# Kernel tuning notes

Hardware: AMD Instinct MI355X
Metric: run time of the kernel (lower is better)

The kernel has to match this reference:

```python
import jax, jax.numpy as jnp
import numpy as np

N = 20000      # total residues (nodes)
E = 320000     # contact edges
G = 16         # graphs in batch
D_IN = 1280    # ESM embedding dim
H = 256        # hidden channels (1=2=3)
C = 500        # GO classes
EPS = 1e-5


def setup_inputs() -> dict:
    key = jax.random.key(0)
    ks = jax.random.split(key, 16)
    s = 0.02
    return {
        "x": jax.random.normal(ks[0], (N, D_IN), jnp.float32),
        "edge_index": jax.random.randint(ks[1], (2, E), 0, N, jnp.int32),
        "edge_attr": jax.random.uniform(ks[2], (E, 1), jnp.float32),
        "batch": jnp.sort(jax.random.randint(ks[3], (N,), 0, G, jnp.int32)),
        "seq_emb": jax.random.normal(ks[4], (G, D_IN), jnp.float32),
        "W1": jax.random.normal(ks[5], (D_IN, H), jnp.float32) * s,
        "b1": jnp.zeros((H,), jnp.float32),
        "g1": jnp.ones((H,), jnp.float32),
        "be1": jnp.zeros((H,), jnp.float32),
        "W2": jax.random.normal(ks[6], (H, H), jnp.float32) * s,
        "b2": jnp.zeros((H,), jnp.float32),
        "g2": jnp.ones((H,), jnp.float32),
        "be2": jnp.zeros((H,), jnp.float32),
        "W3": jax.random.normal(ks[7], (H, H), jnp.float32) * s,
        "b3": jnp.zeros((H,), jnp.float32),
        "g3": jnp.ones((H,), jnp.float32),
        "be3": jnp.zeros((H,), jnp.float32),
        "fc1_w": jax.random.normal(ks[8], (D_IN, H), jnp.float32) * s,
        "fc1_b": jnp.zeros((H,), jnp.float32),
        "lin_w": jax.random.normal(ks[9], (H, C), jnp.float32) * s,
        "lin_b": jnp.zeros((C,), jnp.float32),
    }


def gcn_conv(x, row, col, ew, W, b):
    # PyG GCNConv: x' = D^{-1/2} (A + I) D^{-1/2} X W + b, with edge weights,
    # self-loops of weight 1, aggregation at target (col).
    xw = x @ W                                             # [N, H]
    deg = jax.ops.segment_sum(ew, col, num_segments=N) + 1.0
    dinv = jax.lax.rsqrt(deg)                              # [N]
    norm = dinv[row] * ew * dinv[col]                      # [E]
    agg = jax.ops.segment_sum(norm[:, None] * xw[row], col, num_segments=N)
    agg = agg + (dinv * dinv)[:, None] * xw                # self-loop term
    return agg + b


def batch_norm(x, g, b):
    # training-mode BN over the node dimension (biased variance, as torch)
    m = jnp.mean(x, axis=0)
    v = jnp.var(x, axis=0)
    return (x - m) * jax.lax.rsqrt(v + EPS) * g + b


def reference(x, edge_index, edge_attr, batch, seq_emb,
              W1, b1, g1, be1, W2, b2, g2, be2, W3, b3, g3, be3,
              fc1_w, fc1_b, lin_w, lin_b):
    row, col = edge_index[0], edge_index[1]
    ew = edge_attr[:, 0]

    h = batch_norm(jax.nn.relu(gcn_conv(x, row, col, ew, W1, b1)), g1, be1)
    h = batch_norm(jax.nn.relu(gcn_conv(h, row, col, ew, W2, b2)), g2, be2)
    h = batch_norm(gcn_conv(h, row, col, ew, W3, b3), g3, be3)

    # global_mean_pool over graphs
    sums = jax.ops.segment_sum(h, batch, num_segments=G)        # [G, H]
    cnt = jax.ops.segment_sum(jnp.ones((h.shape[0],), h.dtype), batch, num_segments=G)
    pooled = sums / jnp.maximum(cnt, 1.0)[:, None]

    y = seq_emb @ fc1_w + fc1_b                                 # [G, H]
    out = pooled + y
    # dropout skipped (eval mode)
    out = out @ lin_w + lin_b                                   # [G, C]
    return jax.nn.sigmoid(out)
```

## Files before the change

### kernel.cpp

```cpp
#include <hip/hip_runtime.h>
#include <hip/hip_bf16.h>
#include <math.h>

#define Nn 20000
#define En 320000
#define Gn 16
#define DINn 1280
#define Hn 256
#define Cn 500
#define EPSn 1e-5f
#define BNB 1024
#define SCB 256
#define SNB ((Nn + SCB - 1) / SCB)

typedef __attribute__((ext_vector_type(8))) short bf16x8;
typedef __attribute__((ext_vector_type(4))) float f32x4;

__device__ __forceinline__ float b2f(ushort u) {
    return __uint_as_float(((unsigned int)u) << 16);
}
__device__ __forceinline__ ushort f2b(float f) {
    __hip_bfloat16 h = __float2bfloat16(f);
    return *reinterpret_cast<ushort*>(&h);
}

#define GLOAD16(g, l) __builtin_amdgcn_global_load_lds( \
    (const __attribute__((address_space(1))) unsigned int*)(g), \
    (__attribute__((address_space(3))) unsigned int*)(l), 16, 0, 0)


__global__ void k_deg(const int* col, const float* ew, float* deg) {
    int e = blockIdx.x * blockDim.x + threadIdx.x;
    if (e < En) atomicAdd(&deg[col[e]], ew[e]);
}

__global__ void k_dinv(const float* deg, float* dinv, float* dinv2) {
    int i = blockIdx.x * blockDim.x + threadIdx.x;
    if (i < Nn) {
        float d = deg[i] + 1.0f;
        float r = rsqrtf(d);
        dinv[i] = r;
        dinv2[i] = 1.0f / d;
    }
}

__global__ void k_norm_count(const int* row, const int* col, const float* ew,
                             const float* dinv, float* normE, int* counts) {
    int e = blockIdx.x * blockDim.x + threadIdx.x;
    if (e < En) {
        int r = row[e], c = col[e];
        normE[e] = dinv[r] * ew[e] * dinv[c];
        atomicAdd(&counts[c], 1);
    }
}


__global__ __launch_bounds__(SCB) void k_scanA(const int* __restrict__ counts,
                                               int* __restrict__ excl,
                                               int* __restrict__ blocksum) {
    __shared__ int sd[SCB];
    int t = threadIdx.x, b = blockIdx.x;
    int i = b * SCB + t;
    int v = (i < Nn) ? counts[i] : 0;
    sd[t] = v;
    __syncthreads();
    #pragma unroll
    for (int o = 1; o < SCB; o <<= 1) {
        int tv = (t >= o) ? sd[t - o] : 0;
        __syncthreads();
        sd[t] += tv;
        __syncthreads();
    }
    if (i < Nn) excl[i] = sd[t] - v;
    if (t == SCB - 1) blocksum[b] = sd[t];
}

__global__ __launch_bounds__(128) void k_scanB(const int* __restrict__ blocksum,
                                               int* __restrict__ blockoff,
                                               int* __restrict__ offsets) {
    __shared__ int sd[128];
    int t = threadIdx.x;
    int v = (t < SNB) ? blocksum[t] : 0;
    sd[t] = v;
    __syncthreads();
    #pragma unroll
    for (int o = 1; o < 128; o <<= 1) {
        int tv = (t >= o) ? sd[t - o] : 0;
        __syncthreads();
        sd[t] += tv;
        __syncthreads();
    }
    if (t < SNB) blockoff[t] = sd[t] - v;
    if (t == SNB - 1) offsets[Nn] = sd[t];
}

__global__ __launch_bounds__(SCB) void k_scanC(const int* __restrict__ excl,
                                               const int* __restrict__ blockoff,
                                               int* __restrict__ offsets,
                                               int* __restrict__ cursor) {
    int b = blockIdx.x;
    int i = b * SCB + threadIdx.x;
    if (i < Nn) {
        int o = excl[i] + blockoff[b];
        offsets[i] = o;
        cursor[i] = o;
    }
}

__global__ void k_fill(const int* row, const int* col, const float* normE,
                       int* cursor, int* csr_row, float* csr_w) {
    int e = blockIdx.x * blockDim.x + threadIdx.x;
    if (e < En) {
        int c = col[e];
        int p = atomicAdd(&cursor[c], 1);
        csr_row[p] = row[e];
        csr_w[p] = normE[e];
    }
}


__global__ void k_gbounds(const int* __restrict__ batch, int* __restrict__ gstart) {
    int i = blockIdx.x * blockDim.x + threadIdx.x;
    if (i >= Nn) return;
    int b = batch[i];
    if (i == 0) {
        for (int g = 0; g <= b; g++) gstart[g] = 0;
    } else {
        int pb = batch[i - 1];
        for (int g = pb + 1; g <= b; g++) gstart[g] = i;
    }
    if (i == Nn - 1) {
        for (int g = b + 1; g <= Gn; g++) gstart[g] = Nn;
    }
}


__global__ __launch_bounds__(256) void k_x2bf(const float* __restrict__ x,
                                              ushort* __restrict__ xb) {
    size_t i = ((size_t)blockIdx.x * blockDim.x + threadIdx.x) * 8;
    const float4* xp = reinterpret_cast<const float4*>(&x[i]);
    float4 a = xp[0], b = xp[1];
    ushort t[8];
    t[0] = f2b(a.x); t[1] = f2b(a.y); t[2] = f2b(a.z); t[3] = f2b(a.w);
    t[4] = f2b(b.x); t[5] = f2b(b.y); t[6] = f2b(b.z); t[7] = f2b(b.w);
    *reinterpret_cast<uint4*>(&xb[i]) = *reinterpret_cast<uint4*>(&t[0]);
}


__global__ __launch_bounds__(256) void k_wt(const float* __restrict__ W,
                                            ushort* __restrict__ WT, int K) {
    __shared__ float tile[32][33];
    int k0 = blockIdx.x * 32, n0 = blockIdx.y * 32;
    int tx = threadIdx.x, ty = threadIdx.y;
    #pragma unroll
    for (int i = 0; i < 32; i += 8)
        tile[ty + i][tx] = W[(size_t)(k0 + ty + i) * Hn + n0 + tx];
    __syncthreads();
    #pragma unroll
    for (int i = 0; i < 32; i += 8)
        WT[(size_t)(n0 + ty + i) * K + k0 + tx] = f2b(tile[tx][ty + i]);
}


__global__ __launch_bounds__(256) void k_wtb(const float* __restrict__ W,
                                             const float* __restrict__ scaleA,
                                             const float* __restrict__ shiftA,
                                             ushort* __restrict__ WT,
                                             float* __restrict__ bv) {
    __shared__ float tile[32][33];
    int k0 = blockIdx.x * 32, n0 = blockIdx.y * 32;
    int tx = threadIdx.x, ty = threadIdx.y;
    #pragma unroll
    for (int i = 0; i < 32; i += 8)
        tile[ty + i][tx] = W[(size_t)(k0 + ty + i) * Hn + n0 + tx];
    __syncthreads();
    float sc = scaleA[k0 + tx], sh = shiftA[k0 + tx];
    #pragma unroll
    for (int i = 0; i < 32; i += 8) {
        float w = tile[tx][ty + i];
        WT[(size_t)(n0 + ty + i) * Hn + k0 + tx] = f2b(w * sc);
        float pb = w * sh;
        #pragma unroll
        for (int o = 16; o > 0; o >>= 1) pb += __shfl_down(pb, o, 32);
        if (tx == 0) atomicAdd(&bv[n0 + ty + i], pb);
    }
}


#define GBM 64
#define GBN 128
#define GBK 64

__global__ __launch_bounds__(256) void k_gemm_bf(
    const ushort* __restrict__ A, const ushort* __restrict__ BT,
    ushort* __restrict__ C, int M, int K, int NBL)
{
    __shared__ ushort Asl[GBM][GBK];
    __shared__ ushort Bsl[GBN][GBK];
    const int id = blockIdx.x;
    const int k8 = id >> 3;
    const int r8 = id & 7;
    const int p = (k8 >> 1) * 8 + r8;
    const int bnk = k8 & 1;
    if (p >= NBL) return;
    const int bm = p * GBM;
    const int bn = bnk * GBN;
    const int tid = threadIdx.x;
    const int lane = tid & 63;
    const int wid = tid >> 6;
    const int wm = wid >> 1, wn = wid & 1;
    const int l15 = lane & 15, l16 = lane >> 4;

    const int lrow = lane >> 3;
    const int lcolb = 16 * ((lane & 7) ^ lrow);

    f32x4 acc[2][4] = {};
    const int nt = K / GBK;

    for (int t = 0; t < nt; t++) {
        const int k0 = t * GBK;
        #pragma unroll
        for (int c = 0; c < 2; c++) {
            int chunk = wid * 2 + c;
            int grow = bm + chunk * 8 + lrow;
            if (grow >= M) grow = M - 1;
            const char* src = (const char*)&A[(size_t)grow * K + k0] + lcolb;
            GLOAD16(src, &Asl[chunk * 8][0]);
        }
        #pragma unroll
        for (int c = 0; c < 4; c++) {
            int chunk = wid * 4 + c;
            int grow = bn + chunk * 8 + lrow;
            const char* src = (const char*)&BT[(size_t)grow * K + k0] + lcolb;
            GLOAD16(src, &Bsl[chunk * 8][0]);
        }
        __syncthreads();

        #pragma unroll
        for (int ks = 0; ks < 2; ks++) {
            bf16x8 afr[2], bfr[4];
            #pragma unroll
            for (int i = 0; i < 2; i++) {
                int r = wm * 32 + i * 16 + l15;
                int cb = (ks * 64 + l16 * 16) ^ ((r & 7) << 4);
                afr[i] = *reinterpret_cast<const bf16x8*>((const char*)&Asl[r][0] + cb);
            }
            #pragma unroll
            for (int j = 0; j < 4; j++) {
                int r = wn * 64 + j * 16 + l15;
                int cb = (ks * 64 + l16 * 16) ^ ((r & 7) << 4);
                bfr[j] = *reinterpret_cast<const bf16x8*>((const char*)&Bsl[r][0] + cb);
            }
            #pragma unroll
            for (int i = 0; i < 2; i++)
                #pragma unroll
                for (int j = 0; j < 4; j++)
                    acc[i][j] = __builtin_amdgcn_mfma_f32_16x16x32_bf16(afr[i], bfr[j], acc[i][j], 0, 0, 0);
        }
        __syncthreads();
    }

    #pragma unroll
    for (int i = 0; i < 2; i++) {
        #pragma unroll
        for (int r = 0; r < 4; r++) {
            int grow = bm + wm * 32 + i * 16 + l16 * 4 + r;
            if (grow < M) {
                #pragma unroll
                for (int j = 0; j < 4; j++)
                    C[(size_t)grow * Hn + bn + wn * 64 + j * 16 + l15] = f2b(acc[i][j][r]);
            }
        }
    }
}


__device__ __forceinline__ void agg_accum(float* acc, float w, const uint4& v) {
    unsigned int u;
    u = v.x; acc[0] += w * b2f((ushort)u); acc[1] += w * b2f((ushort)(u >> 16));
    u = v.y; acc[2] += w * b2f((ushort)u); acc[3] += w * b2f((ushort)(u >> 16));
    u = v.z; acc[4] += w * b2f((ushort)u); acc[5] += w * b2f((ushort)(u >> 16));
    u = v.w; acc[6] += w * b2f((ushort)u); acc[7] += w * b2f((ushort)(u >> 16));
}

__global__ __launch_bounds__(256) void k_agg(const ushort* __restrict__ xw,
                                             const int* __restrict__ offsets,
                                             const int* __restrict__ csr_row,
                                             const float* __restrict__ csr_w,
                                             const float* __restrict__ dinv2,
                                             const float* __restrict__ bias,
                                             const float* __restrict__ bv,
                                             ushort* __restrict__ outp, int do_relu) {
    int node = blockIdx.x * 8 + (threadIdx.x >> 5);
    int l32 = threadIdx.x & 31;
    int s = offsets[node], e = offsets[node + 1];
    const uint4* xw4 = reinterpret_cast<const uint4*>(xw);

    float acc[8] = {};
    float wsum = 0.f;
    int k = s;
    for (; k + 4 <= e; k += 4) {
        int r0 = csr_row[k],     r1 = csr_row[k + 1];
        int r2 = csr_row[k + 2], r3 = csr_row[k + 3];
        float w0 = csr_w[k],     w1 = csr_w[k + 1];
        float w2 = csr_w[k + 2], w3 = csr_w[k + 3];
        uint4 v0 = xw4[(size_t)r0 * 32 + l32];
        uint4 v1 = xw4[(size_t)r1 * 32 + l32];
        uint4 v2 = xw4[(size_t)r2 * 32 + l32];
        uint4 v3 = xw4[(size_t)r3 * 32 + l32];
        wsum += (w0 + w1) + (w2 + w3);
        agg_accum(acc, w0, v0);
        agg_accum(acc, w1, v1);
        agg_accum(acc, w2, v2);
        agg_accum(acc, w3, v3);
    }
    for (; k < e; k++) {
        int r = csr_row[k];
        float w = csr_w[k];
        uint4 v = xw4[(size_t)r * 32 + l32];
        wsum += w;
        agg_accum(acc, w, v);
    }
    float d2 = dinv2[node];
    wsum += d2;
    uint4 vs = xw4[(size_t)node * 32 + l32];
    agg_accum(acc, d2, vs);

    const float4* bp = reinterpret_cast<const float4*>(&bias[l32 * 8]);
    float4 bb0 = bp[0], bb1 = bp[1];
    acc[0] += bb0.x; acc[1] += bb0.y; acc[2] += bb0.z; acc[3] += bb0.w;
    acc[4] += bb1.x; acc[5] += bb1.y; acc[6] += bb1.z; acc[7] += bb1.w;
    if (bv) {
        const float4* vp = reinterpret_cast<const float4*>(&bv[l32 * 8]);
        float4 bv0 = vp[0], bv1 = vp[1];
        acc[0] += wsum * bv0.x; acc[1] += wsum * bv0.y;
        acc[2] += wsum * bv0.z; acc[3] += wsum * bv0.w;
        acc[4] += wsum * bv1.x; acc[5] += wsum * bv1.y;
        acc[6] += wsum * bv1.z; acc[7] += wsum * bv1.w;
    }
    if (do_relu) {
        #pragma unroll
        for (int q = 0; q < 8; q++) acc[q] = fmaxf(acc[q], 0.f);
    }
    uint4 o;
    o.x = (unsigned int)f2b(acc[0]) | ((unsigned int)f2b(acc[1]) << 16);
    o.y = (unsigned int)f2b(acc[2]) | ((unsigned int)f2b(acc[3]) << 16);
    o.z = (unsigned int)f2b(acc[4]) | ((unsigned int)f2b(acc[5]) << 16);
    o.w = (unsigned int)f2b(acc[6]) | ((unsigned int)f2b(acc[7]) << 16);
    reinterpret_cast<uint4*>(outp)[(size_t)node * 32 + l32] = o;
}


__global__ __launch_bounds__(256) void k_bnpart(const ushort* __restrict__ h,
                                                float* __restrict__ partial) {
    int f = threadIdx.x;
    int blk = blockIdx.x;
    float s = 0.0f, ss = 0.0f;
    for (int i = blk; i < Nn; i += BNB) {
        float v = b2f(h[(size_t)i * Hn + f]);
        s += v;
        ss += v * v;
    }
    partial[(size_t)blk * 512 + f] = s;
    partial[(size_t)blk * 512 + 256 + f] = ss;
}

__global__ __launch_bounds__(256) void k_bnred(const float* __restrict__ partial,
                                               float* __restrict__ p2) {
    int f = threadIdx.x;
    int b = blockIdx.x;
    int b0 = b * 64;
    float s = 0.0f, ss = 0.0f;
    for (int j = 0; j < 64; j++) {
        const float* p = &partial[(size_t)(b0 + j) * 512];
        s += p[f];
        ss += p[256 + f];
    }
    p2[b * 512 + f] = s;
    p2[b * 512 + 256 + f] = ss;
}

__global__ void k_bnfinal2(const float* __restrict__ p2, const float* g, const float* be,
                           float* scaleA, float* shiftA) {
    int f = threadIdx.x;
    float s = 0.f, ss = 0.f;
    #pragma unroll
    for (int j = 0; j < 16; j++) {
        s += p2[j * 512 + f];
        ss += p2[j * 512 + 256 + f];
    }
    float mean = s / (float)Nn;
    float var = ss / (float)Nn - mean * mean;
    float a = g[f] * rsqrtf(var + EPSn);
    scaleA[f] = a;
    shiftA[f] = be[f] - mean * a;
}


#define PCH 32

__global__ __launch_bounds__(256) void k_pool2(const ushort* __restrict__ h,
                                               const int* __restrict__ gstart,
                                               const float* __restrict__ scaleA,
                                               const float* __restrict__ shiftA,
                                               float* __restrict__ pooled) {
    int g = blockIdx.x;
    int chunk = blockIdx.y;
    int f = threadIdx.x;
    int s = gstart[g], e = gstart[g + 1];
    int len = e - s;
    if (len <= 0) return;
    int per = (len + PCH - 1) / PCH;
    int cs = s + chunk * per;
    int ce = cs + per; if (ce > e) ce = e;
    if (cs >= ce) return;
    float sc = scaleA[f], sh = shiftA[f];
    float acc = 0.0f;
    for (int i = cs; i < ce; i++)
        acc += b2f(h[(size_t)i * Hn + f]) * sc + sh;
    atomicAdd(&pooled[g * Hn + f], acc);
}


__global__ __launch_bounds__(256) void k_head1part(const float* __restrict__ seq_emb,
                                                   const float* __restrict__ fc1_w,
                                                   float* __restrict__ hpart) {
    int g = blockIdx.x;
    int kc = blockIdx.y;
    int j = threadIdx.x;
    const float* se = &seq_emb[(size_t)g * DINn + kc * 128];
    const float* w = &fc1_w[(size_t)kc * 128 * Hn + j];
    float acc = 0.0f;
    #pragma unroll 8
    for (int k = 0; k < 128; k++)
        acc += se[k] * w[(size_t)k * Hn];
    hpart[((size_t)g * 10 + kc) * Hn + j] = acc;
}

__global__ __launch_bounds__(256) void k_head2f(const float* __restrict__ hpart,
                                                const float* __restrict__ fc1_b,
                                                const float* __restrict__ pooled,
                                                const int* __restrict__ gstart,
                                                const float* __restrict__ lin_w,
                                                const float* __restrict__ lin_b,
                                                float* __restrict__ out) {
    __shared__ float pf[Hn];
    int g = blockIdx.x;
    int half = blockIdx.y;
    int j = threadIdx.x;
    float s = fc1_b[j];
    #pragma unroll
    for (int kc = 0; kc < 10; kc++)
        s += hpart[((size_t)g * 10 + kc) * Hn + j];
    float cntf = fmaxf((float)(gstart[g + 1] - gstart[g]), 1.0f);
    pf[j] = pooled[g * Hn + j] / cntf + s;
    __syncthreads();
    int c = half * 250 + j;
    if (j < 250) {
        float a2 = lin_b[c];
        #pragma unroll 8
        for (int k = 0; k < Hn; k++)
            a2 += pf[k] * lin_w[(size_t)k * Cn + c];
        out[g * Cn + c] = 1.0f / (1.0f + expf(-a2));
    }
}


extern "C" void kernel_launch(void* const* d_in, const int* in_sizes, int n_in,
                              void* d_out, int out_size, void* d_ws, size_t ws_size,
                              hipStream_t stream) {
    const float* x        = (const float*)d_in[0];
    const int*   eidx     = (const int*)d_in[1];
    const float* eattr    = (const float*)d_in[2];
    const int*   batch    = (const int*)d_in[3];
    const float* seq_emb  = (const float*)d_in[4];
    const float* W1 = (const float*)d_in[5];
    const float* b1 = (const float*)d_in[6];
    const float* g1 = (const float*)d_in[7];
    const float* be1 = (const float*)d_in[8];
    const float* W2 = (const float*)d_in[9];
    const float* b2 = (const float*)d_in[10];
    const float* g2 = (const float*)d_in[11];
    const float* be2 = (const float*)d_in[12];
    const float* W3 = (const float*)d_in[13];
    const float* b3 = (const float*)d_in[14];
    const float* g3 = (const float*)d_in[15];
    const float* be3 = (const float*)d_in[16];
    const float* fc1_w = (const float*)d_in[17];
    const float* fc1_b = (const float*)d_in[18];
    const float* lin_w = (const float*)d_in[19];
    const float* lin_b = (const float*)d_in[20];
    float* out = (float*)d_out;

    const int* row = eidx;
    const int* col = eidx + En;

    char* ws = (char*)d_ws;
    size_t off = 0;
    auto alloc = [&](size_t bytes) -> char* {
        char* p = ws + off;
        off += (bytes + 255) & ~(size_t)255;
        return p;
    };
    ushort* xb     = (ushort*)alloc((size_t)Nn * DINn * 2);
    ushort* xwb    = (ushort*)alloc((size_t)Nn * Hn * 2);
    ushort* hb     = (ushort*)alloc((size_t)Nn * Hn * 2);
    char*  zbase   = ws + off;
    float* deg     = (float*)alloc(Nn * 4);
    int*   counts  = (int*)alloc(Nn * 4);
    float* bvA     = (float*)alloc(Hn * 4);
    float* bvB     = (float*)alloc(Hn * 4);
    float* pooled  = (float*)alloc(Gn * Hn * 4);
    size_t zspan   = (size_t)((ws + off) - zbase);
    float* dinv    = (float*)alloc(Nn * 4);
    float* dinv2   = (float*)alloc(Nn * 4);
    float* normE   = (float*)alloc(En * 4);
    int*   offsets = (int*)alloc((Nn + 1) * 4);
    int*   cursor  = (int*)alloc(Nn * 4);
    int*   excl    = (int*)alloc(Nn * 4);
    int*   blocksum= (int*)alloc(SNB * 4);
    int*   blockoff= (int*)alloc(SNB * 4);
    int*   csr_row = (int*)alloc(En * 4);
    float* csr_w   = (float*)alloc(En * 4);
    float* scaleA  = (float*)alloc(Hn * 4);
    float* shiftA  = (float*)alloc(Hn * 4);
    int*   gstart  = (int*)alloc((Gn + 1) * 4);
    float* partial = (float*)alloc((size_t)BNB * 512 * 4);
    float* p2      = (float*)alloc(16 * 512 * 4);
    float* hpart   = (float*)alloc((size_t)Gn * 10 * Hn * 4);
    ushort* W1T    = (ushort*)alloc((size_t)Hn * DINn * 2);
    ushort* W2T    = (ushort*)alloc((size_t)Hn * Hn * 2);
    ushort* W3T    = (ushort*)alloc((size_t)Hn * Hn * 2);

    const int TB = 256;
    const int EB = (En + TB - 1) / TB;
    const int NB = (Nn + TB - 1) / TB;

    hipMemsetAsync(zbase, 0, zspan, stream);
    k_deg<<<EB, TB, 0, stream>>>(col, eattr, deg);
    k_dinv<<<NB, TB, 0, stream>>>(deg, dinv, dinv2);
    k_norm_count<<<EB, TB, 0, stream>>>(row, col, eattr, dinv, normE, counts);
    k_scanA<<<SNB, SCB, 0, stream>>>(counts, excl, blocksum);
    k_scanB<<<1, 128, 0, stream>>>(blocksum, blockoff, offsets);
    k_scanC<<<SNB, SCB, 0, stream>>>(excl, blockoff, offsets, cursor);
    k_fill<<<EB, TB, 0, stream>>>(row, col, normE, cursor, csr_row, csr_w);
    k_gbounds<<<NB, TB, 0, stream>>>(batch, gstart);
    k_x2bf<<<(Nn * DINn / 8) / 256, 256, 0, stream>>>(x, xb);
    k_wt<<<dim3(DINn / 32, Hn / 32), dim3(32, 8), 0, stream>>>(W1, W1T, DINn);

    const int NBL = (Nn + GBM - 1) / GBM;
    const int GGRID = ((NBL * 2 + 15) / 16) * 16;
    const int AGB = Nn / 8;

    k_gemm_bf<<<GGRID, 256, 0, stream>>>(xb, W1T, xwb, Nn, DINn, NBL);
    k_agg<<<AGB, 256, 0, stream>>>(xwb, offsets, csr_row, csr_w, dinv2, b1, nullptr, hb, 1);
    k_bnpart<<<BNB, Hn, 0, stream>>>(hb, partial);
    k_bnred<<<16, Hn, 0, stream>>>(partial, p2);
    k_bnfinal2<<<1, Hn, 0, stream>>>(p2, g1, be1, scaleA, shiftA);

    k_wtb<<<dim3(Hn / 32, Hn / 32), dim3(32, 8), 0, stream>>>(W2, scaleA, shiftA, W2T, bvA);
    k_gemm_bf<<<GGRID, 256, 0, stream>>>(hb, W2T, xwb, Nn, Hn, NBL);
    k_agg<<<AGB, 256, 0, stream>>>(xwb, offsets, csr_row, csr_w, dinv2, b2, bvA, hb, 1);
    k_bnpart<<<BNB, Hn, 0, stream>>>(hb, partial);
    k_bnred<<<16, Hn, 0, stream>>>(partial, p2);
    k_bnfinal2<<<1, Hn, 0, stream>>>(p2, g2, be2, scaleA, shiftA);

    k_wtb<<<dim3(Hn / 32, Hn / 32), dim3(32, 8), 0, stream>>>(W3, scaleA, shiftA, W3T, bvB);
    k_gemm_bf<<<GGRID, 256, 0, stream>>>(hb, W3T, xwb, Nn, Hn, NBL);
    k_agg<<<AGB, 256, 0, stream>>>(xwb, offsets, csr_row, csr_w, dinv2, b3, bvB, hb, 0);
    k_bnpart<<<BNB, Hn, 0, stream>>>(hb, partial);
    k_bnred<<<16, Hn, 0, stream>>>(partial, p2);
    k_bnfinal2<<<1, Hn, 0, stream>>>(p2, g3, be3, scaleA, shiftA);

    k_pool2<<<dim3(Gn, PCH), Hn, 0, stream>>>(hb, gstart, scaleA, shiftA, pooled);
    k_head1part<<<dim3(Gn, 10), Hn, 0, stream>>>(seq_emb, fc1_w, hpart);
    k_head2f<<<dim3(Gn, 2), Hn, 0, stream>>>(hpart, fc1_b, pooled, gstart, lin_w, lin_b, out);
}
```

Before: 294.5 us.

## Double-buffer GEMM LDS tiles and fuse degree/count and norm into graph-build kernels

The bf16 MFMA GEMM now holds two LDS buffers. It issues the async global-to-LDS loads for the next K tile before computing on the current one, so load latency can overlap with MFMA work. Graph preprocessing merges the degree and in-edge count atomics into one kernel. It also computes the edge normalisation directly inside the CSR fill kernel, which removes one kernel launch and the normE array round trip. The cost is double the LDS use per GEMM block, which may lower occupancy.

```diff
diff --git a/kernel.cpp b/kernel.cpp
--- a/kernel.cpp
+++ b/kernel.cpp
@@ -29,9 +29,13 @@
     (__attribute__((address_space(3))) unsigned int*)(l), 16, 0, 0)
 
 
-__global__ void k_deg(const int* col, const float* ew, float* deg) {
+__global__ void k_degcnt(const int* col, const float* ew, float* deg, int* counts) {
     int e = blockIdx.x * blockDim.x + threadIdx.x;
-    if (e < En) atomicAdd(&deg[col[e]], ew[e]);
+    if (e < En) {
+        int c = col[e];
+        atomicAdd(&deg[c], ew[e]);
+        atomicAdd(&counts[c], 1);
+    }
 }
 
 __global__ void k_dinv(const float* deg, float* dinv, float* dinv2) {
@@ -41,16 +45,6 @@
         float r = rsqrtf(d);
         dinv[i] = r;
         dinv2[i] = 1.0f / d;
-    }
-}
-
-__global__ void k_norm_count(const int* row, const int* col, const float* ew,
-                             const float* dinv, float* normE, int* counts) {
-    int e = blockIdx.x * blockDim.x + threadIdx.x;
-    if (e < En) {
-        int r = row[e], c = col[e];
-        normE[e] = dinv[r] * ew[e] * dinv[c];
-        atomicAdd(&counts[c], 1);
     }
 }
 
@@ -107,14 +101,15 @@
     }
 }
 
-__global__ void k_fill(const int* row, const int* col, const float* normE,
-                       int* cursor, int* csr_row, float* csr_w) {
+__global__ void k_fill2(const int* row, const int* col, const float* ew,
+                        const float* dinv, int* cursor,
+                        int* csr_row, float* csr_w) {
     int e = blockIdx.x * blockDim.x + threadIdx.x;
     if (e < En) {
-        int c = col[e];
+        int r = row[e], c = col[e];
         int p = atomicAdd(&cursor[c], 1);
-        csr_row[p] = row[e];
-        csr_w[p] = normE[e];
+        csr_row[p] = r;
+        csr_w[p] = dinv[r] * ew[e] * dinv[c];
     }
 }
 
@@ -195,8 +190,8 @@
     const ushort* __restrict__ A, const ushort* __restrict__ BT,
     ushort* __restrict__ C, int M, int K, int NBL)
 {
-    __shared__ ushort Asl[GBM][GBK];
-    __shared__ ushort Bsl[GBN][GBK];
+    __shared__ ushort Asl[2][GBM][GBK];
+    __shared__ ushort Bsl[2][GBN][GBK];
     const int id = blockIdx.x;
     const int k8 = id >> 3;
     const int r8 = id & 7;
@@ -217,7 +212,7 @@
     f32x4 acc[2][4] = {};
     const int nt = K / GBK;
 
-    for (int t = 0; t < nt; t++) {
+    auto STAGE = [&](int buf, int t) {
         const int k0 = t * GBK;
         #pragma unroll
         for (int c = 0; c < 2; c++) {
@@ -225,17 +220,23 @@
             int grow = bm + chunk * 8 + lrow;
             if (grow >= M) grow = M - 1;
             const char* src = (const char*)&A[(size_t)grow * K + k0] + lcolb;
-            GLOAD16(src, &Asl[chunk * 8][0]);
+            GLOAD16(src, &Asl[buf][chunk * 8][0]);
         }
         #pragma unroll
         for (int c = 0; c < 4; c++) {
             int chunk = wid * 4 + c;
             int grow = bn + chunk * 8 + lrow;
             const char* src = (const char*)&BT[(size_t)grow * K + k0] + lcolb;
-            GLOAD16(src, &Bsl[chunk * 8][0]);
+            GLOAD16(src, &Bsl[buf][chunk * 8][0]);
         }
-        __syncthreads();
-
+    };
+
+    STAGE(0, 0);
+    __syncthreads();
+
+    for (int t = 0; t < nt; t++) {
+        const int cur = t & 1;
+        if (t + 1 < nt) STAGE(cur ^ 1, t + 1);
         #pragma unroll
         for (int ks = 0; ks < 2; ks++) {
             bf16x8 afr[2], bfr[4];
@@ -243,13 +244,13 @@
             for (int i = 0; i < 2; i++) {
                 int r = wm * 32 + i * 16 + l15;
                 int cb = (ks * 64 + l16 * 16) ^ ((r & 7) << 4);
-                afr[i] = *reinterpret_cast<const bf16x8*>((const char*)&Asl[r][0] + cb);
+                afr[i] = *reinterpret_cast<const bf16x8*>((const char*)&Asl[cur][r][0] + cb);
             }
             #pragma unroll
             for (int j = 0; j < 4; j++) {
                 int r = wn * 64 + j * 16 + l15;
                 int cb = (ks * 64 + l16 * 16) ^ ((r & 7) << 4);
-                bfr[j] = *reinterpret_cast<const bf16x8*>((const char*)&Bsl[r][0] + cb);
+                bfr[j] = *reinterpret_cast<const bf16x8*>((const char*)&Bsl[cur][r][0] + cb);
             }
             #pragma unroll
             for (int i = 0; i < 2; i++)
@@ -514,7 +515,6 @@
     size_t zspan   = (size_t)((ws + off) - zbase);
     float* dinv    = (float*)alloc(Nn * 4);
     float* dinv2   = (float*)alloc(Nn * 4);
-    float* normE   = (float*)alloc(En * 4);
     int*   offsets = (int*)alloc((Nn + 1) * 4);
     int*   cursor  = (int*)alloc(Nn * 4);
     int*   excl    = (int*)alloc(Nn * 4);
@@ -537,13 +537,12 @@
     const int NB = (Nn + TB - 1) / TB;
 
     hipMemsetAsync(zbase, 0, zspan, stream);
-    k_deg<<<EB, TB, 0, stream>>>(col, eattr, deg);
+    k_degcnt<<<EB, TB, 0, stream>>>(col, eattr, deg, counts);
     k_dinv<<<NB, TB, 0, stream>>>(deg, dinv, dinv2);
-    k_norm_count<<<EB, TB, 0, stream>>>(row, col, eattr, dinv, normE, counts);
     k_scanA<<<SNB, SCB, 0, stream>>>(counts, excl, blocksum);
     k_scanB<<<1, 128, 0, stream>>>(blocksum, blockoff, offsets);
     k_scanC<<<SNB, SCB, 0, stream>>>(excl, blockoff, offsets, cursor);
-    k_fill<<<EB, TB, 0, stream>>>(row, col, normE, cursor, csr_row, csr_w);
+    k_fill2<<<EB, TB, 0, stream>>>(row, col, eattr, dinv, cursor, csr_row, csr_w);
     k_gbounds<<<NB, TB, 0, stream>>>(batch, gstart);
     k_x2bf<<<(Nn * DINn / 8) / 256, 256, 0, stream>>>(x, xb);
     k_wt<<<dim3(DINn / 32, Hn / 32), dim3(32, 8), 0, stream>>>(W1, W1T, DINn);
```

Result: faster. 287.1 us (median of 2 runs) (-2.5%).
